# Optimization experiments

Hardware: AMD Instinct MI355X
Metric: run time of the kernel (lower is better)

## Reference

```python
import jax, jax.numpy as jnp
import numpy as np

N_NODES = 50000
NEG_SLOPE = 0.2

def _leaky(x):
    return jnp.where(x > 0, x, NEG_SLOPE * x)

def _magic_conv(h, src, dst, edge_attr, anet_W, anet_b, mlp_W, mlp_b, eps):
    # align edge features to node dim: [E, d_in]
    e = edge_attr @ anet_W + anet_b
    # message: relu(x_j + edge), gather from source nodes
    msg = jax.nn.relu(h[src] + e)
    # scatter-add aggregate to target nodes: [N, d_in]
    agg = jax.ops.segment_sum(msg, dst, num_segments=N_NODES)
    # GIN-style update: cat([agg, (1+eps)*x]) -> Linear -> LeakyReLU(0.2)
    z = jnp.concatenate([agg, (1.0 + eps) * h], axis=-1) @ mlp_W + mlp_b
    return _leaky(z)

def setup_inputs() -> dict:
    key = jax.random.key(0)
    ks = jax.random.split(key, 16)
    E, D, DE = 800000, 128, 64
    inp = {
        "x": jax.random.normal(ks[0], (N_NODES, D), dtype=jnp.float32),
        "edge_index": jax.random.randint(ks[1], (2, E), 0, N_NODES, dtype=jnp.int64),
        "edge_attr": jax.random.normal(ks[2], (E, DE), dtype=jnp.float32),
    }
    s = lambda d: 1.0 / np.sqrt(d)
    # conv layer 0 (128 -> 128) and layer 1 (128 -> 128)
    for l, k0 in [(0, 3), (1, 8)]:
        inp[f"anet_W{l}"] = jax.random.uniform(ks[k0], (DE, D), jnp.float32, -s(DE), s(DE))
        inp[f"anet_b{l}"] = jax.random.uniform(ks[k0 + 1], (D,), jnp.float32, -s(DE), s(DE))
        inp[f"mlp_W{l}"] = jax.random.uniform(ks[k0 + 2], (2 * D, D), jnp.float32, -s(2 * D), s(2 * D))
        inp[f"mlp_b{l}"] = jax.random.uniform(ks[k0 + 3], (D,), jnp.float32, -s(2 * D), s(2 * D))
        inp[f"eps{l}"] = jnp.full((1,), 1e-4, dtype=jnp.float32)
    # link predictor: Linear(128->128) + LeakyReLU, Linear(128->2)
    inp["lp_W1"] = jax.random.uniform(ks[13], (D, D), jnp.float32, -s(D), s(D))
    inp["lp_b1"] = jax.random.uniform(ks[14], (D,), jnp.float32, -s(D), s(D))
    inp["lp_W2"] = jax.random.uniform(ks[15], (D, 2), jnp.float32, -s(D), s(D))
    inp["lp_b2"] = jnp.zeros((2,), dtype=jnp.float32)
    return inp

def reference(x, edge_index, edge_attr, anet_W0, anet_b0, mlp_W0, mlp_b0, eps0,
              anet_W1, anet_b1, mlp_W1, mlp_b1, eps1,
              lp_W1, lp_b1, lp_W2, lp_b2):
    src = edge_index[0]
    dst = edge_index[1]
    h = _magic_conv(x, src, dst, edge_attr, anet_W0, anet_b0, mlp_W0, mlp_b0, eps0)
    h = _magic_conv(h, src, dst, edge_attr, anet_W1, anet_b1, mlp_W1, mlp_b1, eps1)
    h = jax.nn.relu(h)
    # MULT embed reduction over edge endpoints: [E, 128]
    h_edge = h[src] * h[dst]
    z = _leaky(h_edge @ lp_W1 + lp_b1)
    logits = z @ lp_W2 + lp_b2
    yhat = jax.nn.softmax(logits, axis=-1)
    return (h_edge, yhat)
```

## Files before the change

kernel.cpp:

```cpp
#include <hip/hip_runtime.h>
#include <math.h>

#define NNODES 50000
#define DIM 128
#define DEDGE 64

typedef __attribute__((ext_vector_type(8))) short bf16x8;
typedef __attribute__((ext_vector_type(4))) float f32x4;
typedef __attribute__((ext_vector_type(2))) float f32x2;

__device__ __forceinline__ float bf_lo(unsigned u) { return __builtin_bit_cast(float, u << 16); }
__device__ __forceinline__ float bf_hi(unsigned u) { return __builtin_bit_cast(float, u & 0xFFFF0000u); }
__device__ __forceinline__ float bf_s(short s) {
    return __builtin_bit_cast(float, ((unsigned)(unsigned short)s) << 16);
}
__device__ __forceinline__ unsigned short f2b_rtn(float f) {
    unsigned u = __builtin_bit_cast(unsigned, f);
    u += 0x7FFFu + ((u >> 16) & 1u);
    return (unsigned short)(u >> 16);
}

__global__ void detect_mode_kernel(const void* __restrict__ ei, int* __restrict__ flag) {
    __shared__ int bad;
    if (threadIdx.x == 0) bad = 0;
    __syncthreads();
    const long long* p = (const long long*)ei;
    int localbad = 0;
    for (int i = threadIdx.x; i < 4096; i += blockDim.x) {
        long long v = p[i];
        if (v < 0 || v >= NNODES) localbad = 1;
    }
    if (localbad) atomicOr(&bad, 1);
    __syncthreads();
    if (threadIdx.x == 0) *flag = bad ? 0 : 1;
}

__device__ __forceinline__ int load_idx(const void* ei, long long pos, int mode64) {
    if (mode64) return (int)((const long long*)ei)[pos];
    return ((const int*)ei)[pos];
}

__global__ void prep_weights(const float* __restrict__ aW0, const float* __restrict__ aW1,
                             const float* __restrict__ mW0, const float* __restrict__ mW1,
                             const float* __restrict__ lpW1,
                             const float* __restrict__ eps0p, const float* __restrict__ eps1p,
                             short* __restrict__ wt)
{
    int i = blockIdx.x * 256 + threadIdx.x;
    const float* src; int K, off, f;
    float scale_hi = 1.0f;
    if (i < 8192)        { src = aW0;  K = 64;  off = 0;     f = i; }
    else if (i < 16384)  { src = aW1;  K = 64;  off = 8192;  f = i - 8192; }
    else if (i < 49152)  { src = mW0;  K = 256; off = 16384; f = i - 16384;
                           scale_hi = 1.0f + eps0p[0]; }
    else if (i < 81920)  { src = mW1;  K = 256; off = 49152; f = i - 49152;
                           scale_hi = 1.0f + eps1p[0]; }
    else                 { src = lpW1; K = 128; off = 81920; f = i - 81920; }
    const int NKC = K >> 5;
    int j = f & 7, l = (f >> 3) & 63, c = f >> 9;
    int kc = c % NKC, n = c / NKC;
    int col = n * 16 + (l & 15);
    int k = kc * 32 + ((l >> 4) << 3) + j;
    float v = src[k * DIM + col];
    if (k >= 128) v *= scale_hi;
    wt[off + f] = (short)f2b_rtn(v);
}

__global__ void f32_to_bf16_kernel(const float* __restrict__ in,
                                   unsigned short* __restrict__ out, long long n)
{
    long long i = ((long long)blockIdx.x * 256 + threadIdx.x) * 8;
    if (i >= n) return;
    f32x4 a = *(const f32x4*)(in + i);
    f32x4 b = *(const f32x4*)(in + i + 4);
    unsigned short v[8];
#pragma unroll
    for (int t = 0; t < 4; t++) { v[t] = f2b_rtn(a[t]); v[4 + t] = f2b_rtn(b[t]); }
    unsigned p0 = v[0] | ((unsigned)v[1] << 16);
    unsigned p1 = v[2] | ((unsigned)v[3] << 16);
    unsigned p2 = v[4] | ((unsigned)v[5] << 16);
    unsigned p3 = v[6] | ((unsigned)v[7] << 16);
    f32x4 pk = {__builtin_bit_cast(float, p0), __builtin_bit_cast(float, p1),
                __builtin_bit_cast(float, p2), __builtin_bit_cast(float, p3)};
    *(f32x4*)(out + i) = pk;
}

__global__ void hist_kernel(const void* __restrict__ ei, const int* __restrict__ modep,
                            int* __restrict__ counts, int E)
{
    const int mode64 = *modep;
    for (int e = blockIdx.x * 256 + threadIdx.x; e < E; e += gridDim.x * 256)
        atomicAdd(&counts[load_idx(ei, (long long)E + e, mode64)], 1);
}

__global__ __launch_bounds__(1024) void scan_kernel(const int* __restrict__ counts,
                                                    int* __restrict__ cursor)
{
    __shared__ int part[1024];
    const int t = threadIdx.x;
    const int CH = (NNODES + 1023) / 1024;
    const int lo = t * CH, hi = min(lo + CH, NNODES);
    int s = 0;
    for (int i = lo; i < hi; i++) s += counts[i];
    part[t] = s;
    __syncthreads();
    for (int d = 1; d < 1024; d <<= 1) {
        int v = (t >= d) ? part[t - d] : 0;
        __syncthreads();
        part[t] += v;
        __syncthreads();
    }
    int run = (t == 0) ? 0 : part[t - 1];
    for (int i = lo; i < hi; i++) { cursor[i] = run; run += counts[i]; }
}

__global__ void scatter_kernel(const void* __restrict__ ei, const int* __restrict__ modep,
                               int* __restrict__ cursor, int* __restrict__ perm,
                               int* __restrict__ srcs, int* __restrict__ dsts, int E)
{
    const int mode64 = *modep;
    for (int e = blockIdx.x * 256 + threadIdx.x; e < E; e += gridDim.x * 256) {
        int d = load_idx(ei, (long long)E + e, mode64);
        int s = load_idx(ei, e, mode64);
        int pos = atomicAdd(&cursor[d], 1);
        perm[pos] = e;
        srcs[pos] = s;
        dsts[pos] = d;
    }
}

__global__ void eattr_sort_bf16(const float* __restrict__ eattr, const int* __restrict__ perm,
                                unsigned short* __restrict__ out, int E)
{
    long long i = ((long long)blockIdx.x * 256 + threadIdx.x) * 8;
    if (i >= (long long)E * DEDGE) return;
    long long pos = i >> 6;
    int k = (int)(i & 63);
    long long eid = perm[pos];
    f32x4 a = *(const f32x4*)(eattr + eid * DEDGE + k);
    f32x4 b = *(const f32x4*)(eattr + eid * DEDGE + k + 4);
    unsigned short v[8];
#pragma unroll
    for (int t = 0; t < 4; t++) { v[t] = f2b_rtn(a[t]); v[4 + t] = f2b_rtn(b[t]); }
    unsigned p0 = v[0] | ((unsigned)v[1] << 16);
    unsigned p1 = v[2] | ((unsigned)v[3] << 16);
    unsigned p2 = v[4] | ((unsigned)v[5] << 16);
    unsigned p3 = v[6] | ((unsigned)v[7] << 16);
    f32x4 pk = {__builtin_bit_cast(float, p0), __builtin_bit_cast(float, p1),
                __builtin_bit_cast(float, p2), __builtin_bit_cast(float, p3)};
    __builtin_nontemporal_store(pk, (f32x4*)(out + i));
}

__global__ __launch_bounds__(256, 4) void edge_msg_sorted(
    const unsigned short* __restrict__ hb, const unsigned short* __restrict__ eattrs,
    const int* __restrict__ srcs, const int* __restrict__ dsts,
    const short* __restrict__ Wb,
    const float* __restrict__ bvec, float* __restrict__ agg, int E)
{
    __shared__ float e_lds[4][16][132];
    const int lane = threadIdx.x & 63;
    const int w = threadIdx.x >> 6;
    const int lg = lane >> 4, lr = lane & 15;
    const long long p0 = ((long long)blockIdx.x * 4 + w) * 32;
    if (p0 >= E) return;

    float bias0 = bvec[0 * 16 + lr], bias1 = bvec[1 * 16 + lr],
          bias2 = bvec[2 * 16 + lr], bias3 = bvec[3 * 16 + lr],
          bias4 = bvec[4 * 16 + lr], bias5 = bvec[5 * 16 + lr],
          bias6 = bvec[6 * 16 + lr], bias7 = bvec[7 * 16 + lr];
    float bias[8] = {bias0, bias1, bias2, bias3, bias4, bias5, bias6, bias7};

    float a0 = 0.f, a1 = 0.f;
    int prev = -1;

    const bool fullwave = (p0 + 32 <= E);

#pragma unroll
    for (int st = 0; st < 2; st++) {
        const long long t0 = p0 + st * 16;
        if (t0 >= E) break;
        const long long pos = (t0 + lr < E) ? (t0 + lr) : (E - 1);
        const int sidx = srcs[pos];
        const int didx = dsts[pos];

        f32x4 acc[8];
#pragma unroll
        for (int n = 0; n < 8; n++) {
            float b = bias[n];
            acc[n] = (f32x4){b, b, b, b};
        }
        bf16x8 a[2];
#pragma unroll
        for (int kc = 0; kc < 2; kc++)
            a[kc] = __builtin_nontemporal_load(
                (const bf16x8*)(eattrs + pos * DEDGE + kc * 32 + lg * 8));

#pragma unroll
        for (int n = 0; n < 8; n++) {
#pragma unroll
            for (int kc = 0; kc < 2; kc++) {
                bf16x8 bh = *(const bf16x8*)(Wb + ((n * 2 + kc) * 64 + lane) * 8);
                acc[n] = __builtin_amdgcn_mfma_f32_16x16x32_bf16(a[kc], bh, acc[n], 0, 0, 0);
            }
        }
#pragma unroll
        for (int n = 0; n < 8; n++)
#pragma unroll
            for (int r = 0; r < 4; r++)
                e_lds[w][lg * 4 + r][n * 16 + lr] = acc[n][r];

        if (fullwave) {
            unsigned gu[16];
            int dvs[16];
#pragma unroll
            for (int r = 0; r < 16; r++) {
                int si = __shfl(sidx, r);
                gu[r] = *(const unsigned*)&hb[(long long)si * DIM + 2 * lane];
            }
#pragma unroll
            for (int r = 0; r < 16; r++) dvs[r] = __shfl(didx, r);
#pragma unroll
            for (int r = 0; r < 16; r++) {
                f32x2 ev = *(const f32x2*)&e_lds[w][r][2 * lane];
                float m0 = fmaxf(ev.x + bf_lo(gu[r]), 0.f);
                float m1 = fmaxf(ev.y + bf_hi(gu[r]), 0.f);
                if (dvs[r] != prev && prev >= 0) {
                    float* d = &agg[(long long)prev * DIM + 2 * lane];
                    unsafeAtomicAdd(d, a0);
                    unsafeAtomicAdd(d + 1, a1);
                    a0 = 0.f; a1 = 0.f;
                }
                a0 += m0; a1 += m1; prev = dvs[r];
            }
        } else {
            for (int r = 0; r < 16; r++) {
                if (t0 + r >= E) break;
                int di = __shfl(didx, r);
                int si = __shfl(sidx, r);
                f32x2 ev = *(const f32x2*)&e_lds[w][r][2 * lane];
                unsigned u = *(const unsigned*)&hb[(long long)si * DIM + 2 * lane];
                float m0 = fmaxf(ev.x + bf_lo(u), 0.f);
                float m1 = fmaxf(ev.y + bf_hi(u), 0.f);
                if (di != prev && prev >= 0) {
                    float* d = &agg[(long long)prev * DIM + 2 * lane];
                    unsafeAtomicAdd(d, a0);
                    unsafeAtomicAdd(d + 1, a1);
                    a0 = 0.f; a1 = 0.f;
                }
                a0 += m0; a1 += m1; prev = di;
            }
        }
    }
    if (prev >= 0) {
        float* d = &agg[(long long)prev * DIM + 2 * lane];
        unsafeAtomicAdd(d, a0);
        unsafeAtomicAdd(d + 1, a1);
    }
}

__global__ __launch_bounds__(256, 4) void node_update_mfma(
    const float* __restrict__ agg, const unsigned short* __restrict__ hb,
    const short* __restrict__ Wb, const float* __restrict__ bvec,
    unsigned short* __restrict__ houtb, int relu_flag)
{
    __shared__ float st[4][16][132];
    const int lane = threadIdx.x & 63;
    const int w = threadIdx.x >> 6;
    const int lg = lane >> 4, lr = lane & 15;
    const int n0 = (blockIdx.x * 4 + w) * 16;
    if (n0 >= NNODES) return;
    const int arow = (n0 + lr < NNODES) ? (n0 + lr) : (NNODES - 1);

    f32x4 acc[8];
#pragma unroll
    for (int n = 0; n < 8; n++) {
        float b = bvec[n * 16 + lr];
        acc[n] = (f32x4){b, b, b, b};
    }
#pragma unroll
    for (int kc = 0; kc < 8; kc++) {
        bf16x8 av;
        if (kc < 4) {
            const int k = kc * 32 + lg * 8;
            f32x4 v0 = __builtin_nontemporal_load((const f32x4*)(agg + (long long)arow * DIM + k));
            f32x4 v1 = __builtin_nontemporal_load((const f32x4*)(agg + (long long)arow * DIM + k + 4));
#pragma unroll
            for (int i = 0; i < 4; i++) {
                av[i] = (short)f2b_rtn(v0[i]);
                av[4 + i] = (short)f2b_rtn(v1[i]);
            }
        } else {
            av = *(const bf16x8*)(hb + (long long)arow * DIM + (kc - 4) * 32 + lg * 8);
        }
#pragma unroll
        for (int n = 0; n < 8; n++) {
            bf16x8 bh = *(const bf16x8*)(Wb + ((n * 8 + kc) * 64 + lane) * 8);
            acc[n] = __builtin_amdgcn_mfma_f32_16x16x32_bf16(av, bh, acc[n], 0, 0, 0);
        }
    }
#pragma unroll
    for (int n = 0; n < 8; n++) {
#pragma unroll
        for (int r = 0; r < 4; r++) {
            float z = acc[n][r];
            z = relu_flag ? fmaxf(z, 0.f) : (z > 0.f ? z : 0.2f * z);
            st[w][lg * 4 + r][n * 16 + lr] = z;
        }
    }
    for (int r = 0; r < 16; r++) {
        int row = n0 + r;
        if (row >= NNODES) break;
        f32x2 v = *(const f32x2*)&st[w][r][2 * lane];
        unsigned pk = (unsigned)f2b_rtn(v.x) | ((unsigned)f2b_rtn(v.y) << 16);
        *(unsigned*)&houtb[(long long)row * DIM + 2 * lane] = pk;
    }
}

__global__ __launch_bounds__(256, 6) void edge_head_mfma(
    const unsigned short* __restrict__ hb, const void* __restrict__ ei,
    const int* __restrict__ modep,
    const short* __restrict__ W1b, const float* __restrict__ b1,
    const float* __restrict__ W2, const float* __restrict__ b2,
    float* __restrict__ out_he, float* __restrict__ out_y, int E)
{
    const int mode64 = *modep;
    const int lane = threadIdx.x & 63;
    const int w = threadIdx.x >> 6;
    const int lg = lane >> 4, lr = lane & 15;
    const long long e0 = ((long long)blockIdx.x * 4 + w) * 16;
    if (e0 >= E) return;
    const bool full = (e0 + 16 <= E);
    const long long erow = (full || e0 + lr < E) ? (e0 + lr) : (E - 1);
    int si = load_idx(ei, erow, mode64);
    int di = load_idx(ei, (long long)E + erow, mode64);

    f32x4 acc[8];
#pragma unroll
    for (int n = 0; n < 8; n++) {
        float b = b1[n * 16 + lr];
        acc[n] = (f32x4){b, b, b, b};
    }
    bf16x8 ab[4];
#pragma unroll
    for (int kc = 0; kc < 4; kc++) {
        const int k = kc * 32 + lg * 8;
        bf16x8 hs = *(const bf16x8*)(hb + (long long)si * DIM + k);
        bf16x8 hd = *(const bf16x8*)(hb + (long long)di * DIM + k);
        f32x4 p0, p1;
#pragma unroll
        for (int i = 0; i < 4; i++) {
            p0[i] = bf_s(hs[i]) * bf_s(hd[i]);
            p1[i] = bf_s(hs[4 + i]) * bf_s(hd[4 + i]);
        }
        if (full || e0 + lr < E) {
            __builtin_nontemporal_store(p0, (f32x4*)(out_he + erow * DIM + k));
            __builtin_nontemporal_store(p1, (f32x4*)(out_he + erow * DIM + k + 4));
        }
#pragma unroll
        for (int i = 0; i < 4; i++) {
            ab[kc][i] = (short)f2b_rtn(p0[i]);
            ab[kc][4 + i] = (short)f2b_rtn(p1[i]);
        }
    }
#pragma unroll
    for (int n = 0; n < 8; n++) {
#pragma unroll
        for (int kc = 0; kc < 4; kc++) {
            bf16x8 bh = *(const bf16x8*)(W1b + ((n * 4 + kc) * 64 + lane) * 8);
            acc[n] = __builtin_amdgcn_mfma_f32_16x16x32_bf16(ab[kc], bh, acc[n], 0, 0, 0);
        }
    }
    float q0[4] = {0.f, 0.f, 0.f, 0.f}, q1[4] = {0.f, 0.f, 0.f, 0.f};
#pragma unroll
    for (int n = 0; n < 8; n++) {
        float w2a = W2[(n * 16 + lr) * 2 + 0];
        float w2b = W2[(n * 16 + lr) * 2 + 1];
#pragma unroll
        for (int r = 0; r < 4; r++) {
            float z = acc[n][r];
            z = z > 0.f ? z : 0.2f * z;
            q0[r] = fmaf(z, w2a, q0[r]);
            q1[r] = fmaf(z, w2b, q1[r]);
        }
    }
#pragma unroll
    for (int m = 1; m < 16; m <<= 1) {
#pragma unroll
        for (int r = 0; r < 4; r++) {
            q0[r] += __shfl_xor(q0[r], m);
            q1[r] += __shfl_xor(q1[r], m);
        }
    }
    float c0 = b2[0], c1 = b2[1];
    float s0[4], s1[4];
#pragma unroll
    for (int r = 0; r < 4; r++) {
        float l0 = q0[r] + c0, l1 = q1[r] + c1;
        float mx = fmaxf(l0, l1);
        float x0 = expf(l0 - mx), x1 = expf(l1 - mx);
        float inv = 1.f / (x0 + x1);
        s0[r] = x0 * inv;
        s1[r] = x1 * inv;
    }
    if (full) {
        float ea = (lane & 2) ? s0[1] : s0[0];
        float eb = (lane & 2) ? s0[3] : s0[2];
        float ec = (lane & 2) ? s1[1] : s1[0];
        float ed = (lane & 2) ? s1[3] : s1[2];
        float e0v = (lane & 4) ? eb : ea;
        float e1v = (lane & 4) ? ed : ec;
        float ex = (lane & 1) ? e1v : e0v;
        float v = __shfl(ex, ((lane >> 3) << 4) + (lane & 7));
        if (lane < 32)
            __builtin_nontemporal_store(v, &out_y[e0 * 2 + lane]);
    } else if (lr == 0) {
#pragma unroll
        for (int r = 0; r < 4; r++) {
            long long e = e0 + lg * 4 + r;
            if (e < E) {
                out_y[e * 2 + 0] = s0[r];
                out_y[e * 2 + 1] = s1[r];
            }
        }
    }
}

extern "C" void kernel_launch(void* const* d_in, const int* in_sizes, int n_in,
                              void* d_out, int out_size, void* d_ws, size_t ws_size,
                              hipStream_t stream)
{
    const float* x     = (const float*)d_in[0];
    const void*  ei    = d_in[1];
    const float* eattr = (const float*)d_in[2];
    const float* aW0   = (const float*)d_in[3];
    const float* ab0   = (const float*)d_in[4];
    const float* mW0   = (const float*)d_in[5];
    const float* mb0   = (const float*)d_in[6];
    const float* eps0  = (const float*)d_in[7];
    const float* aW1   = (const float*)d_in[8];
    const float* ab1   = (const float*)d_in[9];
    const float* mW1   = (const float*)d_in[10];
    const float* mb1   = (const float*)d_in[11];
    const float* eps1  = (const float*)d_in[12];
    const float* lpW1  = (const float*)d_in[13];
    const float* lpb1  = (const float*)d_in[14];
    const float* lpW2  = (const float*)d_in[15];
    const float* lpb2  = (const float*)d_in[16];

    const int E = in_sizes[1] / 2;
    const long long NTAB = (long long)NNODES * DIM;

    float* wsf  = (float*)d_ws;
    int*   flag = (int*)d_ws;
    float* agg  = wsf + 64;
    short* wt   = (short*)(agg + NTAB);
    unsigned short* xb_h2b = (unsigned short*)(wt + 98304);
    unsigned short* h1b    = xb_h2b + NTAB;
    int* counts = (int*)(h1b + NTAB);
    int* cursor = counts + 50048;
    int* perm   = cursor + 50048;
    int* srcs   = perm + E;
    int* dsts   = srcs + E;
    unsigned short* eattrs = (unsigned short*)(dsts + E);

    float* out_he = (float*)d_out;
    float* out_y  = out_he + (long long)E * DIM;

    const short* aW0b  = wt;
    const short* aW1b  = wt + 8192;
    const short* mW0b  = wt + 16384;
    const short* mW1b  = wt + 49152;
    const short* lpW1b = wt + 81920;

    detect_mode_kernel<<<1, 256, 0, stream>>>(ei, flag);
    prep_weights<<<384, 256, 0, stream>>>(aW0, aW1, mW0, mW1, lpW1, eps0, eps1, wt);
    f32_to_bf16_kernel<<<(int)(NTAB / 8 / 256), 256, 0, stream>>>(x, xb_h2b, NTAB);

    hipMemsetAsync(counts, 0, 50048 * sizeof(int), stream);
    hist_kernel<<<1024, 256, 0, stream>>>(ei, flag, counts, E);
    scan_kernel<<<1, 1024, 0, stream>>>(counts, cursor);
    scatter_kernel<<<1024, 256, 0, stream>>>(ei, flag, cursor, perm, srcs, dsts, E);
    eattr_sort_bf16<<<(E * DEDGE / 8 + 255) / 256, 256, 0, stream>>>(eattr, perm, eattrs, E);

    const int eblocks32 = (E + 127) / 128;
    const int eblocks16 = (E + 63) / 64;
    const int nblocks = (NNODES + 63) / 64;

    hipMemsetAsync(agg, 0, NTAB * sizeof(float), stream);
    edge_msg_sorted<<<eblocks32, 256, 0, stream>>>(xb_h2b, eattrs, srcs, dsts,
                                                   aW0b, ab0, agg, E);
    node_update_mfma<<<nblocks, 256, 0, stream>>>(agg, xb_h2b, mW0b, mb0, h1b, 0);

    hipMemsetAsync(agg, 0, NTAB * sizeof(float), stream);
    edge_msg_sorted<<<eblocks32, 256, 0, stream>>>(h1b, eattrs, srcs, dsts,
                                                   aW1b, ab1, agg, E);
    node_update_mfma<<<nblocks, 256, 0, stream>>>(agg, h1b, mW1b, mb1, xb_h2b, 1);

    edge_head_mfma<<<eblocks16, 256, 0, stream>>>(xb_h2b, ei, flag, lpW1b, lpb1, lpW2, lpb2,
                                                  out_he, out_y, E);
}
```

Before: 632.1 us.

## Replace atomic scatter aggregation with CSR gather-based per-node aggregation

Splits the edge message step into an edge GEMM kernel that writes bf16 edge messages to a buffer, then a per-node aggregate kernel that walks the CSR row ranges and sums relu(h_src + e) with no atomics. It also replaces the single-block scan with a three-phase multi-block scan that produces rowstart, removes the separate sorted-eattr bf16 pass by reading fp32 edge attributes via perm inside the GEMM, and stores agg in bf16. The aim is to remove float atomics and the agg memsets. In exchange it adds a large E×128 bf16 intermediate write and read per layer, extra bf16 rounding of the messages, and one wave per node, which balances poorly when degrees vary.

```diff
diff --git a/kernel.cpp b/kernel.cpp
--- a/kernel.cpp
+++ b/kernel.cpp
@@ -93,30 +93,51 @@
         atomicAdd(&counts[load_idx(ei, (long long)E + e, mode64)], 1);
 }
 
-__global__ __launch_bounds__(1024) void scan_kernel(const int* __restrict__ counts,
-                                                    int* __restrict__ cursor)
+__global__ __launch_bounds__(1024) void scan1_kernel(const int* __restrict__ counts,
+                                                     int* __restrict__ rowstart,
+                                                     int* __restrict__ bsums)
 {
     __shared__ int part[1024];
     const int t = threadIdx.x;
-    const int CH = (NNODES + 1023) / 1024;
-    const int lo = t * CH, hi = min(lo + CH, NNODES);
-    int s = 0;
-    for (int i = lo; i < hi; i++) s += counts[i];
-    part[t] = s;
+    const int i = blockIdx.x * 1024 + t;
+    int v = (i < NNODES) ? counts[i] : 0;
+    part[t] = v;
     __syncthreads();
     for (int d = 1; d < 1024; d <<= 1) {
-        int v = (t >= d) ? part[t - d] : 0;
+        int u = (t >= d) ? part[t - d] : 0;
         __syncthreads();
-        part[t] += v;
+        part[t] += u;
         __syncthreads();
     }
-    int run = (t == 0) ? 0 : part[t - 1];
-    for (int i = lo; i < hi; i++) { cursor[i] = run; run += counts[i]; }
+    if (i < NNODES) rowstart[i] = part[t] - v;
+    if (t == 1023) bsums[blockIdx.x] = part[1023];
+}
+
+__global__ void scan2_kernel(int* __restrict__ bsums, int nb,
+                             int* __restrict__ rowstart, int E)
+{
+    if (threadIdx.x == 0 && blockIdx.x == 0) {
+        int run = 0;
+        for (int b = 0; b < nb; b++) { int c = bsums[b]; bsums[b] = run; run += c; }
+        rowstart[NNODES] = E;
+    }
+}
+
+__global__ __launch_bounds__(1024) void scan3_kernel(int* __restrict__ rowstart,
+                                                     int* __restrict__ cursor,
+                                                     const int* __restrict__ bsums)
+{
+    const int i = blockIdx.x * 1024 + threadIdx.x;
+    if (i < NNODES) {
+        int v = rowstart[i] + bsums[blockIdx.x];
+        rowstart[i] = v;
+        cursor[i] = v;
+    }
 }
 
 __global__ void scatter_kernel(const void* __restrict__ ei, const int* __restrict__ modep,
                                int* __restrict__ cursor, int* __restrict__ perm,
-                               int* __restrict__ srcs, int* __restrict__ dsts, int E)
+                               int* __restrict__ srcs, int E)
 {
     const int mode64 = *modep;
     for (int e = blockIdx.x * 256 + threadIdx.x; e < E; e += gridDim.x * 256) {
@@ -125,37 +146,13 @@
         int pos = atomicAdd(&cursor[d], 1);
         perm[pos] = e;
         srcs[pos] = s;
-        dsts[pos] = d;
-    }
-}
-
-__global__ void eattr_sort_bf16(const float* __restrict__ eattr, const int* __restrict__ perm,
-                                unsigned short* __restrict__ out, int E)
-{
-    long long i = ((long long)blockIdx.x * 256 + threadIdx.x) * 8;
-    if (i >= (long long)E * DEDGE) return;
-    long long pos = i >> 6;
-    int k = (int)(i & 63);
-    long long eid = perm[pos];
-    f32x4 a = *(const f32x4*)(eattr + eid * DEDGE + k);
-    f32x4 b = *(const f32x4*)(eattr + eid * DEDGE + k + 4);
-    unsigned short v[8];
-#pragma unroll
-    for (int t = 0; t < 4; t++) { v[t] = f2b_rtn(a[t]); v[4 + t] = f2b_rtn(b[t]); }
-    unsigned p0 = v[0] | ((unsigned)v[1] << 16);
-    unsigned p1 = v[2] | ((unsigned)v[3] << 16);
-    unsigned p2 = v[4] | ((unsigned)v[5] << 16);
-    unsigned p3 = v[6] | ((unsigned)v[7] << 16);
-    f32x4 pk = {__builtin_bit_cast(float, p0), __builtin_bit_cast(float, p1),
-                __builtin_bit_cast(float, p2), __builtin_bit_cast(float, p3)};
-    __builtin_nontemporal_store(pk, (f32x4*)(out + i));
-}
-
-__global__ __launch_bounds__(256, 4) void edge_msg_sorted(
-    const unsigned short* __restrict__ hb, const unsigned short* __restrict__ eattrs,
-    const int* __restrict__ srcs, const int* __restrict__ dsts,
-    const short* __restrict__ Wb,
-    const float* __restrict__ bvec, float* __restrict__ agg, int E)
+    }
+}
+
+__global__ __launch_bounds__(256, 4) void edge_gemm(
+    const float* __restrict__ eattr, const int* __restrict__ perm,
+    const short* __restrict__ Wb, const float* __restrict__ bvec,
+    unsigned short* __restrict__ emsg, int E)
 {
     __shared__ float e_lds[4][16][132];
     const int lane = threadIdx.x & 63;
@@ -164,37 +161,35 @@
     const long long p0 = ((long long)blockIdx.x * 4 + w) * 32;
     if (p0 >= E) return;
 
-    float bias0 = bvec[0 * 16 + lr], bias1 = bvec[1 * 16 + lr],
-          bias2 = bvec[2 * 16 + lr], bias3 = bvec[3 * 16 + lr],
-          bias4 = bvec[4 * 16 + lr], bias5 = bvec[5 * 16 + lr],
-          bias6 = bvec[6 * 16 + lr], bias7 = bvec[7 * 16 + lr];
-    float bias[8] = {bias0, bias1, bias2, bias3, bias4, bias5, bias6, bias7};
-
-    float a0 = 0.f, a1 = 0.f;
-    int prev = -1;
-
-    const bool fullwave = (p0 + 32 <= E);
+    float bias[8];
+#pragma unroll
+    for (int n = 0; n < 8; n++) bias[n] = bvec[n * 16 + lr];
 
 #pragma unroll
     for (int st = 0; st < 2; st++) {
         const long long t0 = p0 + st * 16;
         if (t0 >= E) break;
         const long long pos = (t0 + lr < E) ? (t0 + lr) : (E - 1);
-        const int sidx = srcs[pos];
-        const int didx = dsts[pos];
-
+        const long long eid = perm[pos];
+
+        bf16x8 a[2];
+#pragma unroll
+        for (int kc = 0; kc < 2; kc++) {
+            const float* p = eattr + eid * DEDGE + kc * 32 + lg * 8;
+            f32x4 v0 = __builtin_nontemporal_load((const f32x4*)p);
+            f32x4 v1 = __builtin_nontemporal_load((const f32x4*)(p + 4));
+#pragma unroll
+            for (int i = 0; i < 4; i++) {
+                a[kc][i] = (short)f2b_rtn(v0[i]);
+                a[kc][4 + i] = (short)f2b_rtn(v1[i]);
+            }
+        }
         f32x4 acc[8];
 #pragma unroll
         for (int n = 0; n < 8; n++) {
             float b = bias[n];
             acc[n] = (f32x4){b, b, b, b};
         }
-        bf16x8 a[2];
-#pragma unroll
-        for (int kc = 0; kc < 2; kc++)
-            a[kc] = __builtin_nontemporal_load(
-                (const bf16x8*)(eattrs + pos * DEDGE + kc * 32 + lg * 8));
-
 #pragma unroll
         for (int n = 0; n < 8; n++) {
 #pragma unroll
@@ -209,57 +204,41 @@
             for (int r = 0; r < 4; r++)
                 e_lds[w][lg * 4 + r][n * 16 + lr] = acc[n][r];
 
-        if (fullwave) {
-            unsigned gu[16];
-            int dvs[16];
-#pragma unroll
-            for (int r = 0; r < 16; r++) {
-                int si = __shfl(sidx, r);
-                gu[r] = *(const unsigned*)&hb[(long long)si * DIM + 2 * lane];
-            }
-#pragma unroll
-            for (int r = 0; r < 16; r++) dvs[r] = __shfl(didx, r);
-#pragma unroll
-            for (int r = 0; r < 16; r++) {
-                f32x2 ev = *(const f32x2*)&e_lds[w][r][2 * lane];
-                float m0 = fmaxf(ev.x + bf_lo(gu[r]), 0.f);
-                float m1 = fmaxf(ev.y + bf_hi(gu[r]), 0.f);
-                if (dvs[r] != prev && prev >= 0) {
-                    float* d = &agg[(long long)prev * DIM + 2 * lane];
-                    unsafeAtomicAdd(d, a0);
-                    unsafeAtomicAdd(d + 1, a1);
-                    a0 = 0.f; a1 = 0.f;
-                }
-                a0 += m0; a1 += m1; prev = dvs[r];
-            }
-        } else {
-            for (int r = 0; r < 16; r++) {
-                if (t0 + r >= E) break;
-                int di = __shfl(didx, r);
-                int si = __shfl(sidx, r);
-                f32x2 ev = *(const f32x2*)&e_lds[w][r][2 * lane];
-                unsigned u = *(const unsigned*)&hb[(long long)si * DIM + 2 * lane];
-                float m0 = fmaxf(ev.x + bf_lo(u), 0.f);
-                float m1 = fmaxf(ev.y + bf_hi(u), 0.f);
-                if (di != prev && prev >= 0) {
-                    float* d = &agg[(long long)prev * DIM + 2 * lane];
-                    unsafeAtomicAdd(d, a0);
-                    unsafeAtomicAdd(d + 1, a1);
-                    a0 = 0.f; a1 = 0.f;
-                }
-                a0 += m0; a1 += m1; prev = di;
-            }
-        }
-    }
-    if (prev >= 0) {
-        float* d = &agg[(long long)prev * DIM + 2 * lane];
-        unsafeAtomicAdd(d, a0);
-        unsafeAtomicAdd(d + 1, a1);
-    }
+#pragma unroll
+        for (int r = 0; r < 16; r++) {
+            if (t0 + r >= E) break;
+            f32x2 ev = *(const f32x2*)&e_lds[w][r][2 * lane];
+            unsigned pk = (unsigned)f2b_rtn(ev.x) | ((unsigned)f2b_rtn(ev.y) << 16);
+            *(unsigned*)&emsg[(t0 + r) * DIM + 2 * lane] = pk;
+        }
+    }
+}
+
+__global__ __launch_bounds__(256) void aggregate_kernel(
+    const unsigned short* __restrict__ emsg, const unsigned short* __restrict__ hb,
+    const int* __restrict__ srcs, const int* __restrict__ rowstart,
+    unsigned short* __restrict__ aggb)
+{
+    const int lane = threadIdx.x & 63;
+    const int w = threadIdx.x >> 6;
+    const int n = blockIdx.x * 4 + w;
+    if (n >= NNODES) return;
+    const int s = rowstart[n];
+    const int e = rowstart[n + 1];
+    float a0 = 0.f, a1 = 0.f;
+    for (int p = s; p < e; p++) {
+        unsigned ue = *(const unsigned*)&emsg[(long long)p * DIM + 2 * lane];
+        int si = srcs[p];
+        unsigned uh = *(const unsigned*)&hb[(long long)si * DIM + 2 * lane];
+        a0 += fmaxf(bf_lo(ue) + bf_lo(uh), 0.f);
+        a1 += fmaxf(bf_hi(ue) + bf_hi(uh), 0.f);
+    }
+    unsigned pk = (unsigned)f2b_rtn(a0) | ((unsigned)f2b_rtn(a1) << 16);
+    *(unsigned*)&aggb[(long long)n * DIM + 2 * lane] = pk;
 }
 
 __global__ __launch_bounds__(256, 4) void node_update_mfma(
-    const float* __restrict__ agg, const unsigned short* __restrict__ hb,
+    const unsigned short* __restrict__ aggb, const unsigned short* __restrict__ hb,
     const short* __restrict__ Wb, const float* __restrict__ bvec,
     unsigned short* __restrict__ houtb, int relu_flag)
 {
@@ -281,14 +260,7 @@
     for (int kc = 0; kc < 8; kc++) {
         bf16x8 av;
         if (kc < 4) {
-            const int k = kc * 32 + lg * 8;
-            f32x4 v0 = __builtin_nontemporal_load((const f32x4*)(agg + (long long)arow * DIM + k));
-            f32x4 v1 = __builtin_nontemporal_load((const f32x4*)(agg + (long long)arow * DIM + k + 4));
-#pragma unroll
-            for (int i = 0; i < 4; i++) {
-                av[i] = (short)f2b_rtn(v0[i]);
-                av[4 + i] = (short)f2b_rtn(v1[i]);
-            }
+            av = *(const bf16x8*)(aggb + (long long)arow * DIM + kc * 32 + lg * 8);
         } else {
             av = *(const bf16x8*)(hb + (long long)arow * DIM + (kc - 4) * 32 + lg * 8);
         }
@@ -450,18 +422,18 @@
     const int E = in_sizes[1] / 2;
     const long long NTAB = (long long)NNODES * DIM;
 
-    float* wsf  = (float*)d_ws;
     int*   flag = (int*)d_ws;
-    float* agg  = wsf + 64;
-    short* wt   = (short*)(agg + NTAB);
+    short* wt   = (short*)((char*)d_ws + 256);
     unsigned short* xb_h2b = (unsigned short*)(wt + 98304);
     unsigned short* h1b    = xb_h2b + NTAB;
-    int* counts = (int*)(h1b + NTAB);
-    int* cursor = counts + 50048;
-    int* perm   = cursor + 50048;
-    int* srcs   = perm + E;
-    int* dsts   = srcs + E;
-    unsigned short* eattrs = (unsigned short*)(dsts + E);
+    unsigned short* aggb   = h1b + NTAB;
+    unsigned short* emsg   = aggb + NTAB;
+    int* counts   = (int*)(emsg + (long long)E * DIM);
+    int* rowstart = counts + 50048;
+    int* cursor   = rowstart + 50112;
+    int* bsums    = cursor + 50048;
+    int* perm     = bsums + 64;
+    int* srcs     = perm + E;
 
     float* out_he = (float*)d_out;
     float* out_y  = out_he + (long long)E * DIM;
@@ -478,23 +450,24 @@
 
     hipMemsetAsync(counts, 0, 50048 * sizeof(int), stream);
     hist_kernel<<<1024, 256, 0, stream>>>(ei, flag, counts, E);
-    scan_kernel<<<1, 1024, 0, stream>>>(counts, cursor);
-    scatter_kernel<<<1024, 256, 0, stream>>>(ei, flag, cursor, perm, srcs, dsts, E);
-    eattr_sort_bf16<<<(E * DEDGE / 8 + 255) / 256, 256, 0, stream>>>(eattr, perm, eattrs, E);
+    const int sblocks = (NNODES + 1023) / 1024;
+    scan1_kernel<<<sblocks, 1024, 0, stream>>>(counts, rowstart, bsums);
+    scan2_kernel<<<1, 64, 0, stream>>>(bsums, sblocks, rowstart, E);
+    scan3_kernel<<<sblocks, 1024, 0, stream>>>(rowstart, cursor, bsums);
+    scatter_kernel<<<1024, 256, 0, stream>>>(ei, flag, cursor, perm, srcs, E);
 
     const int eblocks32 = (E + 127) / 128;
     const int eblocks16 = (E + 63) / 64;
-    const int nblocks = (NNODES + 63) / 64;
-
-    hipMemsetAsync(agg, 0, NTAB * sizeof(float), stream);
-    edge_msg_sorted<<<eblocks32, 256, 0, stream>>>(xb_h2b, eattrs, srcs, dsts,
-                                                   aW0b, ab0, agg, E);
-    node_update_mfma<<<nblocks, 256, 0, stream>>>(agg, xb_h2b, mW0b, mb0, h1b, 0);
-
-    hipMemsetAsync(agg, 0, NTAB * sizeof(float), stream);
-    edge_msg_sorted<<<eblocks32, 256, 0, stream>>>(h1b, eattrs, srcs, dsts,
-                                                   aW1b, ab1, agg, E);
-    node_update_mfma<<<nblocks, 256, 0, stream>>>(agg, h1b, mW1b, mb1, xb_h2b, 1);
+    const int nblocks   = (NNODES + 63) / 64;
+    const int ablocks   = (NNODES + 3) / 4;
+
+    edge_gemm<<<eblocks32, 256, 0, stream>>>(eattr, perm, aW0b, ab0, emsg, E);
+    aggregate_kernel<<<ablocks, 256, 0, stream>>>(emsg, xb_h2b, srcs, rowstart, aggb);
+    node_update_mfma<<<nblocks, 256, 0, stream>>>(aggb, xb_h2b, mW0b, mb0, h1b, 0);
+
+    edge_gemm<<<eblocks32, 256, 0, stream>>>(eattr, perm, aW1b, ab1, emsg, E);
+    aggregate_kernel<<<ablocks, 256, 0, stream>>>(emsg, h1b, srcs, rowstart, aggb);
+    node_update_mfma<<<nblocks, 256, 0, stream>>>(aggb, h1b, mW1b, mb1, xb_h2b, 1);
 
     edge_head_mfma<<<eblocks16, 256, 0, stream>>>(xb_h2b, ei, flag, lpW1b, lpb1, lpW2, lpb2,
                                                   out_he, out_y, E);
```

Result: slower. 735.1 us (+16.3%).

## Parallelize prefix scan across blocks and process two edge tiles per head wave

Applied to the files above, without the earlier changes.

The single-block serial-chunk scan over node counts becomes a three-kernel parallel block scan: per-block scans, a serial scan of the block sums, then an add-back pass. Separately, the edge head kernel now handles two 16-edge tiles per wave, so bias and W2 loads are hoisted and done once, and half as many blocks are launched. The first change removes a long single-block serial pass but adds two extra kernel launches. The second cuts per-wave setup cost at the price of fewer waves in flight for latency hiding.

```diff
diff --git a/kernel.cpp b/kernel.cpp
--- a/kernel.cpp
+++ b/kernel.cpp
@@ -93,25 +93,39 @@
         atomicAdd(&counts[load_idx(ei, (long long)E + e, mode64)], 1);
 }
 
-__global__ __launch_bounds__(1024) void scan_kernel(const int* __restrict__ counts,
-                                                    int* __restrict__ cursor)
+__global__ __launch_bounds__(1024) void scan1_kernel(const int* __restrict__ counts,
+                                                     int* __restrict__ cursor,
+                                                     int* __restrict__ bsums)
 {
     __shared__ int part[1024];
     const int t = threadIdx.x;
-    const int CH = (NNODES + 1023) / 1024;
-    const int lo = t * CH, hi = min(lo + CH, NNODES);
-    int s = 0;
-    for (int i = lo; i < hi; i++) s += counts[i];
-    part[t] = s;
+    const int i = blockIdx.x * 1024 + t;
+    int v = (i < NNODES) ? counts[i] : 0;
+    part[t] = v;
     __syncthreads();
     for (int d = 1; d < 1024; d <<= 1) {
-        int v = (t >= d) ? part[t - d] : 0;
+        int u = (t >= d) ? part[t - d] : 0;
         __syncthreads();
-        part[t] += v;
+        part[t] += u;
         __syncthreads();
     }
-    int run = (t == 0) ? 0 : part[t - 1];
-    for (int i = lo; i < hi; i++) { cursor[i] = run; run += counts[i]; }
+    if (i < NNODES) cursor[i] = part[t] - v;
+    if (t == 1023) bsums[blockIdx.x] = part[1023];
+}
+
+__global__ void scan2_kernel(int* __restrict__ bsums, int nb)
+{
+    if (threadIdx.x == 0 && blockIdx.x == 0) {
+        int run = 0;
+        for (int b = 0; b < nb; b++) { int c = bsums[b]; bsums[b] = run; run += c; }
+    }
+}
+
+__global__ __launch_bounds__(1024) void scan3_kernel(int* __restrict__ cursor,
+                                                     const int* __restrict__ bsums)
+{
+    const int i = blockIdx.x * 1024 + threadIdx.x;
+    if (i < NNODES) cursor[i] += bsums[blockIdx.x];
 }
 
 __global__ void scatter_kernel(const void* __restrict__ ei, const int* __restrict__ modep,
@@ -164,15 +178,12 @@
     const long long p0 = ((long long)blockIdx.x * 4 + w) * 32;
     if (p0 >= E) return;
 
-    float bias0 = bvec[0 * 16 + lr], bias1 = bvec[1 * 16 + lr],
-          bias2 = bvec[2 * 16 + lr], bias3 = bvec[3 * 16 + lr],
-          bias4 = bvec[4 * 16 + lr], bias5 = bvec[5 * 16 + lr],
-          bias6 = bvec[6 * 16 + lr], bias7 = bvec[7 * 16 + lr];
-    float bias[8] = {bias0, bias1, bias2, bias3, bias4, bias5, bias6, bias7};
+    float bias[8];
+#pragma unroll
+    for (int n = 0; n < 8; n++) bias[n] = bvec[n * 16 + lr];
 
     float a0 = 0.f, a1 = 0.f;
     int prev = -1;
-
     const bool fullwave = (p0 + 32 <= E);
 
 #pragma unroll
@@ -327,99 +338,111 @@
     const int lane = threadIdx.x & 63;
     const int w = threadIdx.x >> 6;
     const int lg = lane >> 4, lr = lane & 15;
-    const long long e0 = ((long long)blockIdx.x * 4 + w) * 16;
-    if (e0 >= E) return;
-    const bool full = (e0 + 16 <= E);
-    const long long erow = (full || e0 + lr < E) ? (e0 + lr) : (E - 1);
-    int si = load_idx(ei, erow, mode64);
-    int di = load_idx(ei, (long long)E + erow, mode64);
-
-    f32x4 acc[8];
+    const long long base = ((long long)blockIdx.x * 4 + w) * 32;
+    if (base >= E) return;
+
+    float bias[8], w2a[8], w2b[8];
 #pragma unroll
     for (int n = 0; n < 8; n++) {
-        float b = b1[n * 16 + lr];
-        acc[n] = (f32x4){b, b, b, b};
-    }
-    bf16x8 ab[4];
-#pragma unroll
-    for (int kc = 0; kc < 4; kc++) {
-        const int k = kc * 32 + lg * 8;
-        bf16x8 hs = *(const bf16x8*)(hb + (long long)si * DIM + k);
-        bf16x8 hd = *(const bf16x8*)(hb + (long long)di * DIM + k);
-        f32x4 p0, p1;
-#pragma unroll
-        for (int i = 0; i < 4; i++) {
-            p0[i] = bf_s(hs[i]) * bf_s(hd[i]);
-            p1[i] = bf_s(hs[4 + i]) * bf_s(hd[4 + i]);
-        }
-        if (full || e0 + lr < E) {
-            __builtin_nontemporal_store(p0, (f32x4*)(out_he + erow * DIM + k));
-            __builtin_nontemporal_store(p1, (f32x4*)(out_he + erow * DIM + k + 4));
-        }
-#pragma unroll
-        for (int i = 0; i < 4; i++) {
-            ab[kc][i] = (short)f2b_rtn(p0[i]);
-            ab[kc][4 + i] = (short)f2b_rtn(p1[i]);
-        }
-    }
-#pragma unroll
-    for (int n = 0; n < 8; n++) {
+        bias[n] = b1[n * 16 + lr];
+        w2a[n] = W2[(n * 16 + lr) * 2 + 0];
+        w2b[n] = W2[(n * 16 + lr) * 2 + 1];
+    }
+    const float c0 = b2[0], c1 = b2[1];
+
+#pragma unroll
+    for (int st = 0; st < 2; st++) {
+        const long long e0 = base + st * 16;
+        if (e0 >= E) break;
+        const bool full = (e0 + 16 <= E);
+        const long long erow = (full || e0 + lr < E) ? (e0 + lr) : (E - 1);
+        int si = load_idx(ei, erow, mode64);
+        int di = load_idx(ei, (long long)E + erow, mode64);
+
+        f32x4 acc[8];
+#pragma unroll
+        for (int n = 0; n < 8; n++) {
+            float b = bias[n];
+            acc[n] = (f32x4){b, b, b, b};
+        }
+        bf16x8 ab[4];
 #pragma unroll
         for (int kc = 0; kc < 4; kc++) {
-            bf16x8 bh = *(const bf16x8*)(W1b + ((n * 4 + kc) * 64 + lane) * 8);
-            acc[n] = __builtin_amdgcn_mfma_f32_16x16x32_bf16(ab[kc], bh, acc[n], 0, 0, 0);
-        }
-    }
-    float q0[4] = {0.f, 0.f, 0.f, 0.f}, q1[4] = {0.f, 0.f, 0.f, 0.f};
-#pragma unroll
-    for (int n = 0; n < 8; n++) {
-        float w2a = W2[(n * 16 + lr) * 2 + 0];
-        float w2b = W2[(n * 16 + lr) * 2 + 1];
+            const int k = kc * 32 + lg * 8;
+            bf16x8 hs = *(const bf16x8*)(hb + (long long)si * DIM + k);
+            bf16x8 hd = *(const bf16x8*)(hb + (long long)di * DIM + k);
+            f32x4 p0, p1;
+#pragma unroll
+            for (int i = 0; i < 4; i++) {
+                p0[i] = bf_s(hs[i]) * bf_s(hd[i]);
+                p1[i] = bf_s(hs[4 + i]) * bf_s(hd[4 + i]);
+            }
+            if (full || e0 + lr < E) {
+                __builtin_nontemporal_store(p0, (f32x4*)(out_he + erow * DIM + k));
+                __builtin_nontemporal_store(p1, (f32x4*)(out_he + erow * DIM + k + 4));
+            }
+#pragma unroll
+            for (int i = 0; i < 4; i++) {
+                ab[kc][i] = (short)f2b_rtn(p0[i]);
+                ab[kc][4 + i] = (short)f2b_rtn(p1[i]);
+            }
+        }
+#pragma unroll
+        for (int n = 0; n < 8; n++) {
+#pragma unroll
+            for (int kc = 0; kc < 4; kc++) {
+                bf16x8 bh = *(const bf16x8*)(W1b + ((n * 4 + kc) * 64 + lane) * 8);
+                acc[n] = __builtin_amdgcn_mfma_f32_16x16x32_bf16(ab[kc], bh, acc[n], 0, 0, 0);
+            }
+        }
+        float q0[4] = {0.f, 0.f, 0.f, 0.f}, q1[4] = {0.f, 0.f, 0.f, 0.f};
+#pragma unroll
+        for (int n = 0; n < 8; n++) {
+#pragma unroll
+            for (int r = 0; r < 4; r++) {
+                float z = acc[n][r];
+                z = z > 0.f ? z : 0.2f * z;
+                q0[r] = fmaf(z, w2a[n], q0[r]);
+                q1[r] = fmaf(z, w2b[n], q1[r]);
+            }
+        }
+#pragma unroll
+        for (int m = 1; m < 16; m <<= 1) {
+#pragma unroll
+            for (int r = 0; r < 4; r++) {
+                q0[r] += __shfl_xor(q0[r], m);
+                q1[r] += __shfl_xor(q1[r], m);
+            }
+        }
+        float s0[4], s1[4];
 #pragma unroll
         for (int r = 0; r < 4; r++) {
-            float z = acc[n][r];
-            z = z > 0.f ? z : 0.2f * z;
-            q0[r] = fmaf(z, w2a, q0[r]);
-            q1[r] = fmaf(z, w2b, q1[r]);
-        }
-    }
-#pragma unroll
-    for (int m = 1; m < 16; m <<= 1) {
-#pragma unroll
-        for (int r = 0; r < 4; r++) {
-            q0[r] += __shfl_xor(q0[r], m);
-            q1[r] += __shfl_xor(q1[r], m);
-        }
-    }
-    float c0 = b2[0], c1 = b2[1];
-    float s0[4], s1[4];
-#pragma unroll
-    for (int r = 0; r < 4; r++) {
-        float l0 = q0[r] + c0, l1 = q1[r] + c1;
-        float mx = fmaxf(l0, l1);
-        float x0 = expf(l0 - mx), x1 = expf(l1 - mx);
-        float inv = 1.f / (x0 + x1);
-        s0[r] = x0 * inv;
-        s1[r] = x1 * inv;
-    }
-    if (full) {
-        float ea = (lane & 2) ? s0[1] : s0[0];
-        float eb = (lane & 2) ? s0[3] : s0[2];
-        float ec = (lane & 2) ? s1[1] : s1[0];
-        float ed = (lane & 2) ? s1[3] : s1[2];
-        float e0v = (lane & 4) ? eb : ea;
-        float e1v = (lane & 4) ? ed : ec;
-        float ex = (lane & 1) ? e1v : e0v;
-        float v = __shfl(ex, ((lane >> 3) << 4) + (lane & 7));
-        if (lane < 32)
-            __builtin_nontemporal_store(v, &out_y[e0 * 2 + lane]);
-    } else if (lr == 0) {
-#pragma unroll
-        for (int r = 0; r < 4; r++) {
-            long long e = e0 + lg * 4 + r;
-            if (e < E) {
-                out_y[e * 2 + 0] = s0[r];
-                out_y[e * 2 + 1] = s1[r];
+            float l0 = q0[r] + c0, l1 = q1[r] + c1;
+            float mx = fmaxf(l0, l1);
+            float x0 = expf(l0 - mx), x1 = expf(l1 - mx);
+            float inv = 1.f / (x0 + x1);
+            s0[r] = x0 * inv;
+            s1[r] = x1 * inv;
+        }
+        if (full) {
+            float ea = (lane & 2) ? s0[1] : s0[0];
+            float eb = (lane & 2) ? s0[3] : s0[2];
+            float ec = (lane & 2) ? s1[1] : s1[0];
+            float ed = (lane & 2) ? s1[3] : s1[2];
+            float e0v = (lane & 4) ? eb : ea;
+            float e1v = (lane & 4) ? ed : ec;
+            float ex = (lane & 1) ? e1v : e0v;
+            float v = __shfl(ex, ((lane >> 3) << 4) + (lane & 7));
+            if (lane < 32)
+                __builtin_nontemporal_store(v, &out_y[e0 * 2 + lane]);
+        } else if (lr == 0) {
+#pragma unroll
+            for (int r = 0; r < 4; r++) {
+                long long e = e0 + lg * 4 + r;
+                if (e < E) {
+                    out_y[e * 2 + 0] = s0[r];
+                    out_y[e * 2 + 1] = s1[r];
+                }
             }
         }
     }
@@ -458,7 +481,8 @@
     unsigned short* h1b    = xb_h2b + NTAB;
     int* counts = (int*)(h1b + NTAB);
     int* cursor = counts + 50048;
-    int* perm   = cursor + 50048;
+    int* bsums  = cursor + 50048;
+    int* perm   = bsums + 64;
     int* srcs   = perm + E;
     int* dsts   = srcs + E;
     unsigned short* eattrs = (unsigned short*)(dsts + E);
@@ -478,12 +502,14 @@
 
     hipMemsetAsync(counts, 0, 50048 * sizeof(int), stream);
     hist_kernel<<<1024, 256, 0, stream>>>(ei, flag, counts, E);
-    scan_kernel<<<1, 1024, 0, stream>>>(counts, cursor);
+    const int sblocks = (NNODES + 1023) / 1024;
+    scan1_kernel<<<sblocks, 1024, 0, stream>>>(counts, cursor, bsums);
+    scan2_kernel<<<1, 64, 0, stream>>>(bsums, sblocks);
+    scan3_kernel<<<sblocks, 1024, 0, stream>>>(cursor, bsums);
     scatter_kernel<<<1024, 256, 0, stream>>>(ei, flag, cursor, perm, srcs, dsts, E);
     eattr_sort_bf16<<<(E * DEDGE / 8 + 255) / 256, 256, 0, stream>>>(eattr, perm, eattrs, E);
 
     const int eblocks32 = (E + 127) / 128;
-    const int eblocks16 = (E + 63) / 64;
     const int nblocks = (NNODES + 63) / 64;
 
     hipMemsetAsync(agg, 0, NTAB * sizeof(float), stream);
@@ -496,6 +522,6 @@
                                                    aW1b, ab1, agg, E);
     node_update_mfma<<<nblocks, 256, 0, stream>>>(agg, h1b, mW1b, mb1, xb_h2b, 1);
 
-    edge_head_mfma<<<eblocks16, 256, 0, stream>>>(xb_h2b, ei, flag, lpW1b, lpb1, lpW2, lpb2,
+    edge_head_mfma<<<eblocks32, 256, 0, stream>>>(xb_h2b, ei, flag, lpW1b, lpb1, lpW2, lpb2,
                                                   out_he, out_y, E);
 }
```

Result: slower. 798.4 us (+26.3%).
